# Kernel optimization log

Measured on AMD Instinct MI355X. Metric: run time of the kernel, lower is better.

The kernel has to match this reference:

```python
import jax, jax.numpy as jnp
import numpy as np

ATOM = 8          # atom_size
STRIDE = 4
NB_ATOMS = 256
LMBDA = 0.1       # l1 prox weight (prox_params)
NONDIFF = 20      # nondiff_steps (run under stop_gradient, mirroring torch.no_grad)
DIFF = 5          # diff_steps


def setup_inputs() -> dict:
    key = jax.random.key(0)
    k1, k2 = jax.random.split(key)
    y = jax.random.normal(k1, (8, 3, 256, 256), dtype=jnp.float32)
    # atoms ~ N(0,1)/sqrt(nb_channels*atom_size^2), as in __init__ with init='random'
    atoms = jax.random.normal(k2, (NB_ATOMS, 3, ATOM, ATOM), dtype=jnp.float32) / np.float32(np.sqrt(3 * ATOM * ATOM))
    return {"y": y, "atoms": atoms}


def _forward(y, atoms):
    B, C, H, W = y.shape
    a, s = ATOM, STRIDE
    Hp = (H - a) // s + 1
    Wp = (W - a) // s + 1
    D = C * a * a

    # patch row/col index grids: rows[ph, i] = ph*s + i
    rows = (jnp.arange(Hp) * s)[:, None] + jnp.arange(a)          # [Hp, a]
    cols = (jnp.arange(Wp) * s)[:, None] + jnp.arange(a)          # [Wp, a]
    R4 = rows[:, :, None, None]                                    # [Hp, a, 1, 1]
    C4 = cols[None, None, :, :]                                    # [1, 1, Wp, a]

    # unfold: extract overlapping patches -> [B, C, Hp, a, Wp, a] -> [N, D] (channel-major, matching torch)
    p6 = y[:, :, R4, C4]
    p = p6.transpose(0, 2, 4, 1, 3, 5).reshape(B * Hp * Wp, D)     # N = B*Hp*Wp

    mean = jnp.mean(p, axis=1, keepdims=True)                      # per-patch mean
    p = p - mean

    # l2-normalize atoms
    A = atoms.reshape(NB_ATOMS, D)
    A = A / jnp.linalg.norm(A, axis=1, keepdims=True)              # [nA, D]

    X = A @ A.T                                                    # [nA, nA] Gram matrix
    q = A @ p.T                                                    # [nA, N]
    L = jnp.linalg.norm(X, 2)                                      # spectral norm (Lipschitz const)
    thr = LMBDA / L

    def ista_step(c, _):
        c = c - (X @ c - q) / L
        c = jnp.sign(c) * jnp.maximum(jnp.abs(c) - thr, 0.0)       # soft-threshold prox
        return c, None

    c0 = jnp.zeros((NB_ATOMS, q.shape[1]), dtype=q.dtype)
    c, _ = jax.lax.scan(ista_step, c0, None, length=NONDIFF)
    c = jax.lax.stop_gradient(c)                                    # torch.no_grad() warmup
    c, _ = jax.lax.scan(ista_step, c, None, length=DIFF)

    # reconstruct patches: einsum('ij,il->jl') = c.T @ A, add mean back
    rec = c.T @ A + mean                                            # [N, D]
    p6r = rec.reshape(B, Hp, Wp, C, a, a).transpose(0, 3, 1, 4, 2, 5)  # [B, C, Hp, a, Wp, a]

    # fold: overlap-add patches back to image
    out = jnp.zeros((B, C, H, W), dtype=y.dtype).at[:, :, R4, C4].add(p6r)
    counts = jnp.zeros((H, W), dtype=y.dtype).at[R4, C4].add(
        jnp.ones((Hp, a, Wp, a), dtype=y.dtype))                    # overlap divisors
    return out / counts


def reference(y, atoms):
    return _forward(y, atoms)
```

## Files before the change

kernel.cpp:

```cpp
#include <hip/hip_runtime.h>
#include <math.h>

#define NPATCH 31752
#define TILE   64
#define PSTR   200
#define MSTR   200

typedef _Float16 f16;
typedef __attribute__((ext_vector_type(2))) _Float16 f16x2;
typedef __attribute__((ext_vector_type(4))) _Float16 f16x4;
typedef __attribute__((ext_vector_type(8))) _Float16 f16x8;
typedef __attribute__((ext_vector_type(2))) __fp16   hf16x2;
typedef __attribute__((ext_vector_type(4))) float    f32x4;
#define MFMA16 __builtin_amdgcn_mfma_f32_16x16x32_f16

union HU { f16x2 h; hf16x2 g; unsigned u; };

__device__ __forceinline__ f16x2 pk2(float a, float b)
{
    HU r; r.g = __builtin_amdgcn_cvt_pkrtz(a, b);
    return r.h;
}

__device__ __forceinline__ f16x2 shrink2(f16x2 v, f16x2 thr2)
{
    HU a; a.h = v;
    unsigned sgn = a.u & 0x80008000u;
    a.u &= 0x7FFF7FFFu;
    f16x2 t = a.h - thr2;
    t = __builtin_elementwise_max(t, (f16x2)(f16)0);
    HU r; r.h = t; r.u |= sgn;
    return r.h;
}

__global__ void fusedpack_kernel(const float* __restrict__ atoms,
                                 float* __restrict__ As,
                                 f16* __restrict__ Ap, f16* __restrict__ Ab,
                                 float* __restrict__ out, int out_n)
{
    __shared__ float part[6];
    const int b = blockIdx.x, t = threadIdx.x;
    {
        float4* o4 = (float4*)out;
        int tot4 = out_n >> 2;
        for (int u = b * 192 + t; u < tot4; u += 256 * 192)
            o4[u] = (float4){0.f, 0.f, 0.f, 0.f};
    }
    float v = atoms[b*192 + t];
    float s = v*v, r = v;
    #pragma unroll
    for (int m = 1; m < 64; m <<= 1) { s += __shfl_xor(s, m, 64); r += __shfl_xor(r, m, 64); }
    const int wv = t >> 6, lane = t & 63;
    if (lane == 0) { part[wv] = s; part[3 + wv] = r; }
    __syncthreads();
    s = part[0] + part[1] + part[2];
    r = part[3] + part[4] + part[5];
    float rn = 1.0f / sqrtf(s);
    float a  = v * rn;
    if (t == 0) As[b] = r * rn;
    f16 ah = (f16)a;
    {
        int I = b >> 4, l16 = b & 15;
        int ks = t >> 5, q = (t >> 3) & 3, j = t & 7;
        Ap[(((I*6 + ks)*64) + q*16 + l16)*8 + j] = ah;
    }
    {
        int dt = t >> 4, dl = t & 15;
        int ks = b >> 5, q = (b >> 3) & 3, j = b & 7;
        Ab[(((dt*8 + ks)*64) + q*16 + dl)*8 + j] = ah;
    }
    (void)lane;
}

__global__ __launch_bounds__(512, 1)
void lchain_kernel(const f16* __restrict__ Ab, const f16* __restrict__ Ap,
                   f16* __restrict__ Xp, float* __restrict__ scal)
{
    __shared__ __align__(16) f16 mls[2 * 192 * MSTR];
    __shared__ float red[8];
    __shared__ float trc[16];
    const int tid = threadIdx.x, bid = blockIdx.x;
    const int wv = tid >> 6, lane = tid & 63;
    const int quad = lane >> 4, l16 = lane & 15;

    if (bid > 0) {
        const int I = bid - 1;
        const f16x8* ApV = (const f16x8*)Ap;
        #pragma unroll
        for (int jj = 0; jj < 2; ++jj) {
            int J = wv*2 + jj;
            f32x4 acc = (f32x4){0,0,0,0};
            #pragma unroll
            for (int ks = 0; ks < 6; ++ks) {
                f16x8 af = ApV[(I*6 + ks)*64 + lane];
                f16x8 bf = ApV[(J*6 + ks)*64 + lane];
                acc = MFMA16(af, bf, acc, 0, 0, 0);
            }
            f16x2 lo = pk2(acc[0], acc[1]);
            f16x2 hi = pk2(acc[2], acc[3]);
            f16x4 cc; cc[0]=lo[0]; cc[1]=lo[1]; cc[2]=hi[0]; cc[3]=hi[1];
            int ks2 = I >> 1;
            int q2  = (2*I + (quad >> 1)) & 3;
            int j2  = (quad & 1) * 4;
            *(f16x4*)&Xp[(((J*8 + ks2)*64) + q2*16 + l16)*8 + j2] = cc;
        }
        return;
    }

    const int g3 = (wv >> 1) * 3;
    const int h6 = (wv & 1) * 6;
    const f16x8* AbV = (const f16x8*)Ab;

    f32x4 acc[3][6];
    #pragma unroll
    for (int it = 0; it < 3; ++it)
        #pragma unroll
        for (int jj = 0; jj < 6; ++jj) acc[it][jj] = (f32x4){0,0,0,0};
    for (int ks = 0; ks < 8; ++ks) {
        f16x8 bf[6];
        #pragma unroll
        for (int jj = 0; jj < 6; ++jj) bf[jj] = AbV[((h6 + jj)*8 + ks)*64 + lane];
        #pragma unroll
        for (int it = 0; it < 3; ++it) {
            f16x8 af = AbV[((g3 + it)*8 + ks)*64 + lane];
            #pragma unroll
            for (int jj = 0; jj < 6; ++jj)
                acc[it][jj] = MFMA16(af, bf[jj], acc[it][jj], 0, 0, 0);
        }
    }
    #pragma unroll
    for (int it = 0; it < 3; ++it) {
        int I = g3 + it;
        #pragma unroll
        for (int jj = 0; jj < 6; ++jj) {
            int J = h6 + jj;
            f16x2 lo = pk2(acc[it][jj][0], acc[it][jj][1]);
            f16x2 hi = pk2(acc[it][jj][2], acc[it][jj][3]);
            f16x4 cc; cc[0]=lo[0]; cc[1]=lo[1]; cc[2]=hi[0]; cc[3]=hi[1];
            *(f16x4*)&mls[(J*16 + l16)*MSTR + I*16 + quad*4] = cc;
        }
    }
    __syncthreads();

    float rprev = 1.0f;
    for (int t = 1; t <= 8; ++t) {
        const f16* src = mls + ((t & 1) ^ 1) * (192 * MSTR);
        f16*       dst = mls + (t & 1) * (192 * MSTR);
        const float inv = 1.0f / rprev;
        const float inv2 = inv * inv;

        f32x4 a2[3][6];
        #pragma unroll
        for (int it = 0; it < 3; ++it)
            #pragma unroll
            for (int jj = 0; jj < 6; ++jj) a2[it][jj] = (f32x4){0,0,0,0};
        for (int ksd = 0; ksd < 6; ++ksd) {
            f16x8 bf[6];
            #pragma unroll
            for (int jj = 0; jj < 6; ++jj)
                bf[jj] = *(const f16x8*)&src[((h6 + jj)*16 + l16)*MSTR + ksd*32 + quad*8];
            #pragma unroll
            for (int it = 0; it < 3; ++it) {
                f16x8 af = *(const f16x8*)&src[((g3 + it)*16 + l16)*MSTR + ksd*32 + quad*8];
                #pragma unroll
                for (int jj = 0; jj < 6; ++jj)
                    a2[it][jj] = MFMA16(af, bf[jj], a2[it][jj], 0, 0, 0);
            }
        }
        float dsum = 0.0f;
        #pragma unroll
        for (int it = 0; it < 3; ++it) {
            int I = g3 + it;
            #pragma unroll
            for (int jj = 0; jj < 6; ++jj) {
                int J = h6 + jj;
                float v0 = a2[it][jj][0] * inv2;
                float v1 = a2[it][jj][1] * inv2;
                float v2 = a2[it][jj][2] * inv2;
                float v3 = a2[it][jj][3] * inv2;
                f16x2 lo = pk2(v0, v1);
                f16x2 hi = pk2(v2, v3);
                f16x4 cc; cc[0]=lo[0]; cc[1]=lo[1]; cc[2]=hi[0]; cc[3]=hi[1];
                *(f16x4*)&dst[(J*16 + l16)*MSTR + I*16 + quad*4] = cc;
                if (J == I) {
                    int dg = l16 - quad*4;
                    if (dg >= 0 && dg < 4)
                        dsum += (dg == 0 ? v0 : dg == 1 ? v1 : dg == 2 ? v2 : v3);
                }
            }
        }
        #pragma unroll
        for (int m = 1; m < 64; m <<= 1) dsum += __shfl_xor(dsum, m, 64);
        if (lane == 0) red[wv] = dsum;
        __syncthreads();
        float r = red[0] + red[1] + red[2] + red[3]
                + red[4] + red[5] + red[6] + red[7];
        if (tid == 0) trc[t] = r;
        rprev = r;
        __syncthreads();
    }
    if (tid == 0) {
        float a = 0.0f;
        #pragma unroll
        for (int u = 1; u <= 8; ++u) a += exp2f(-(float)u) * log2f(trc[u]);
        float L = exp2f(a);
        scal[16] = 1.0f / L;
        scal[17] = 0.1f / L;
    }
}

__global__ __launch_bounds__(512, 4)
void mega_kernel(const float* __restrict__ y,
                 const f16* __restrict__ Xp, const f16* __restrict__ Ap,
                 const f16* __restrict__ Ab, const float* __restrict__ As,
                 const float* __restrict__ scal, float* __restrict__ out)
{
    __shared__ f16      p_lds[TILE * PSTR];
    __shared__ f16      c_lds[2 * 16 * 512];
    __shared__ float    mean_lds[TILE];
    __shared__ unsigned pco[TILE];

    const int tid  = threadIdx.x;
    const int base = blockIdx.x * TILE;
    const int wv = tid >> 6, lane = tid & 63, quad = lane >> 4, l16 = lane & 15;
    const float invL = scal[16];
    const float thr  = scal[17];
    const f16x2 thr2 = { (f16)thr, (f16)thr };

    #define CWADDR(st, rt, ct) \
        ((st)*8192 + ((ct)*8 + wv)*512 \
         + (((rt)*2 + (quad>>1))*16 + l16)*8 + (quad&1)*4)
    #define LDB0(st, ks) (*(const f16x8*)&c_lds[(st)*8192 + (ks)*512 + lane*8])
    #define LDB1(st, ks) (*(const f16x8*)&c_lds[(st)*8192 + (8 + (ks))*512 + lane*8])

    f16x8 greg[2][8];
    {
        const f16x8* XpV = (const f16x8*)Xp;
        #pragma unroll
        for (int rt = 0; rt < 2; ++rt) {
            int r = (wv*2 + rt)*16 + l16;
            #pragma unroll
            for (int ks = 0; ks < 8; ++ks) {
                f16x8 xv = XpV[((wv*2 + rt)*8 + ks)*64 + lane];
                float f[8];
                #pragma unroll
                for (int j = 0; j < 8; ++j) {
                    int c = ks*32 + quad*8 + j;
                    float d = (r == c) ? 1.0f : 0.0f;
                    f[j] = fmaf(-invL, (float)xv[j], d);
                }
                f16x2 p0 = pk2(f[0], f[1]), p1 = pk2(f[2], f[3]);
                f16x2 p2 = pk2(f[4], f[5]), p3 = pk2(f[6], f[7]);
                f16x8 gg;
                gg[0]=p0[0]; gg[1]=p0[1]; gg[2]=p1[0]; gg[3]=p1[1];
                gg[4]=p2[0]; gg[5]=p2[1]; gg[6]=p3[0]; gg[7]=p3[1];
                greg[rt][ks] = gg;
            }
        }
    }

    {
        int n_l = tid >> 3, qq = tid & 7;
        int n = base + n_l; if (n >= NPATCH) n = NPATCH - 1;
        int b = n / 3969, rem = n - b * 3969;
        int r = rem / 63, sc = rem - r * 63;
        float s = 0.0f;
        #pragma unroll
        for (int u = 0; u < 3; ++u) {
            int d  = qq * 24 + u * 8;
            int ch = d >> 6, id = (d & 63) >> 3;
            const float* src = &y[((b*3 + ch)*256 + (r*4 + id))*256 + sc*4];
            float4 a = *(const float4*)src;
            float4 bq = *(const float4*)(src + 4);
            s += a.x + a.y + a.z + a.w + bq.x + bq.y + bq.z + bq.w;
            f16x8 h = { (f16)a.x, (f16)a.y, (f16)a.z, (f16)a.w,
                        (f16)bq.x, (f16)bq.y, (f16)bq.z, (f16)bq.w };
            *(f16x8*)&p_lds[n_l * PSTR + d] = h;
        }
        s += __shfl_xor(s, 1, 64);
        s += __shfl_xor(s, 2, 64);
        s += __shfl_xor(s, 4, 64);
        if (qq == 0) {
            mean_lds[n_l] = s * (1.0f / 192.0f);
            pco[n_l] = ((unsigned)b << 16) | ((unsigned)r << 8) | (unsigned)sc;
        }
    }
    __syncthreads();

    f16x2 qslo[2][2][2], qshi[2][2][2];
    const f16x8* ApV = (const f16x8*)Ap;
    #pragma unroll
    for (int st = 0; st < 2; ++st) {
        f32x4 qf[2][2];
        #pragma unroll
        for (int rt = 0; rt < 2; ++rt)
            #pragma unroll
            for (int ct = 0; ct < 2; ++ct) qf[rt][ct] = (f32x4){0,0,0,0};
        #pragma unroll
        for (int ks = 0; ks < 6; ++ks) {
            f16x8 bf[2];
            #pragma unroll
            for (int ct = 0; ct < 2; ++ct)
                bf[ct] = *(const f16x8*)&p_lds[(st*32 + ct*16 + l16)*PSTR + ks*32 + quad*8];
            #pragma unroll
            for (int rt = 0; rt < 2; ++rt) {
                f16x8 af = ApV[((wv*2 + rt)*6 + ks)*64 + lane];
                #pragma unroll
                for (int ct = 0; ct < 2; ++ct)
                    qf[rt][ct] = MFMA16(af, bf[ct], qf[rt][ct], 0, 0, 0);
            }
        }
        #pragma unroll
        for (int rt = 0; rt < 2; ++rt) {
            float4 av = *(const float4*)&As[(wv*2 + rt)*16 + quad*4];
            #pragma unroll
            for (int ct = 0; ct < 2; ++ct) {
                float mn = mean_lds[st*32 + ct*16 + l16];
                float q0 = (qf[rt][ct][0] - mn*av.x) * invL;
                float q1 = (qf[rt][ct][1] - mn*av.y) * invL;
                float q2 = (qf[rt][ct][2] - mn*av.z) * invL;
                float q3 = (qf[rt][ct][3] - mn*av.w) * invL;
                f16x2 lo = pk2(q0, q1);
                f16x2 hi = pk2(q2, q3);
                qslo[st][rt][ct] = lo;  qshi[st][rt][ct] = hi;
                f16x2 clo = shrink2(lo, thr2);
                f16x2 chi = shrink2(hi, thr2);
                f16x4 cc; cc[0]=clo[0]; cc[1]=clo[1]; cc[2]=chi[0]; cc[3]=chi[1];
                *(f16x4*)&c_lds[CWADDR(st, rt, ct)] = cc;
            }
        }
    }
    __syncthreads();

    f16x8 pa0 = LDB0(0,0), pa1 = LDB1(0,0), pa2 = LDB0(0,1), pa3 = LDB1(0,1);
    for (int it = 0; it < 24; ++it) {
        f32x4 af[2][2];
        #pragma unroll
        for (int rt = 0; rt < 2; ++rt)
            #pragma unroll
            for (int ct = 0; ct < 2; ++ct) af[rt][ct] = (f32x4){0,0,0,0};
        __builtin_amdgcn_s_setprio(1);
        #pragma unroll
        for (int ks = 0; ks < 8; ++ks) {
            f16x8 b0 = (ks == 0) ? pa0 : (ks == 1) ? pa2 : LDB0(0, ks);
            f16x8 b1 = (ks == 0) ? pa1 : (ks == 1) ? pa3 : LDB1(0, ks);
            #pragma unroll
            for (int rt = 0; rt < 2; ++rt) {
                af[rt][0] = MFMA16(greg[rt][ks], b0, af[rt][0], 0, 0, 0);
                af[rt][1] = MFMA16(greg[rt][ks], b1, af[rt][1], 0, 0, 0);
            }
        }
        __builtin_amdgcn_s_setprio(0);
        __syncthreads();
        f16x8 pb0 = LDB0(1,0), pb1 = LDB1(1,0), pb2 = LDB0(1,1), pb3 = LDB1(1,1);
        #pragma unroll
        for (int rt = 0; rt < 2; ++rt)
            #pragma unroll
            for (int ct = 0; ct < 2; ++ct) {
                f16x2 vlo = pk2(af[rt][ct][0], af[rt][ct][1]) + qslo[0][rt][ct];
                f16x2 vhi = pk2(af[rt][ct][2], af[rt][ct][3]) + qshi[0][rt][ct];
                vlo = shrink2(vlo, thr2);
                vhi = shrink2(vhi, thr2);
                f16x4 cc; cc[0]=vlo[0]; cc[1]=vlo[1]; cc[2]=vhi[0]; cc[3]=vhi[1];
                *(f16x4*)&c_lds[CWADDR(0, rt, ct)] = cc;
            }
        #pragma unroll
        for (int rt = 0; rt < 2; ++rt)
            #pragma unroll
            for (int ct = 0; ct < 2; ++ct) af[rt][ct] = (f32x4){0,0,0,0};
        __builtin_amdgcn_s_setprio(1);
        #pragma unroll
        for (int ks = 0; ks < 8; ++ks) {
            f16x8 b0 = (ks == 0) ? pb0 : (ks == 1) ? pb2 : LDB0(1, ks);
            f16x8 b1 = (ks == 0) ? pb1 : (ks == 1) ? pb3 : LDB1(1, ks);
            #pragma unroll
            for (int rt = 0; rt < 2; ++rt) {
                af[rt][0] = MFMA16(greg[rt][ks], b0, af[rt][0], 0, 0, 0);
                af[rt][1] = MFMA16(greg[rt][ks], b1, af[rt][1], 0, 0, 0);
            }
        }
        __builtin_amdgcn_s_setprio(0);
        __syncthreads();
        pa0 = LDB0(0,0); pa1 = LDB1(0,0); pa2 = LDB0(0,1); pa3 = LDB1(0,1);
        #pragma unroll
        for (int rt = 0; rt < 2; ++rt)
            #pragma unroll
            for (int ct = 0; ct < 2; ++ct) {
                f16x2 vlo = pk2(af[rt][ct][0], af[rt][ct][1]) + qslo[1][rt][ct];
                f16x2 vhi = pk2(af[rt][ct][2], af[rt][ct][3]) + qshi[1][rt][ct];
                vlo = shrink2(vlo, thr2);
                vhi = shrink2(vhi, thr2);
                f16x4 cc; cc[0]=vlo[0]; cc[1]=vlo[1]; cc[2]=vhi[0]; cc[3]=vhi[1];
                *(f16x4*)&c_lds[CWADDR(1, rt, ct)] = cc;
            }
    }
    __syncthreads();

    const int nt = wv >> 2, dtb = 3 * (wv & 3);
    const f16x8* AbV = (const f16x8*)Ab;
    #pragma unroll
    for (int st = 0; st < 2; ++st) {
        f32x4 rf[3];
        #pragma unroll
        for (int u = 0; u < 3; ++u) rf[u] = (f32x4){0,0,0,0};
        #pragma unroll
        for (int ks = 0; ks < 8; ++ks) {
            f16x8 afr = *(const f16x8*)&c_lds[st*8192 + (nt*8 + ks)*512 + lane*8];
            #pragma unroll
            for (int u = 0; u < 3; ++u) {
                f16x8 bb = AbV[((dtb + u)*8 + ks)*64 + lane];
                rf[u] = MFMA16(afr, bb, rf[u], 0, 0, 0);
            }
        }
        #pragma unroll
        for (int g = 0; g < 4; ++g) {
            int nl = nt*16 + quad*4 + g;
            int n  = base + st*32 + nl;
            if (n < NPATCH) {
                unsigned pc = pco[st*32 + nl];
                int b = pc >> 16, r = (pc >> 8) & 255, sc = pc & 255;
                float mn = mean_lds[st*32 + nl];
                #pragma unroll
                for (int u = 0; u < 3; ++u) {
                    int d  = (dtb + u)*16 + l16;
                    int ch = d >> 6, dh = (d & 63) >> 3, dw = d & 7;
                    int h  = r*4 + dh, w2 = sc*4 + dw;
                    int cnth = min(62, h >> 2)  - (max(h - 4, 0) >> 2) + 1;
                    int cntw = min(62, w2 >> 2) - (max(w2 - 4, 0) >> 2) + 1;
                    float rcp = 1.0f / (float)(cnth * cntw);
                    atomicAdd(&out[((b*3 + ch)*256 + (r*4 + dh))*256 + sc*4 + dw],
                              (rf[u][g] + mn) * rcp);
                }
            }
        }
    }
    #undef CWADDR
    #undef LDB0
    #undef LDB1
}

extern "C" void kernel_launch(void* const* d_in, const int* in_sizes, int n_in,
                              void* d_out, int out_size, void* d_ws, size_t ws_size,
                              hipStream_t stream)
{
    const float* y     = (const float*)d_in[0];
    const float* atoms = (const float*)d_in[1];
    float* out = (float*)d_out;
    float* ws  = (float*)d_ws;

    float* As   = ws + 49152;
    float* scal = ws + 49408;
    f16*   Ap   = (f16*)(ws + 49440);
    f16*   Ab   = (f16*)(ws + 74016);
    f16*   Xp   = (f16*)(ws + 98592);
    int    outn = out_size;

    fusedpack_kernel<<<256, 192, 0, stream>>>(atoms, As, Ap, Ab, out, outn);
    lchain_kernel   <<<17, 512,  0, stream>>>(Ab, Ap, Xp, scal);
    mega_kernel     <<<(NPATCH + TILE - 1) / TILE, 512, 0, stream>>>
        (y, Xp, Ap, Ab, As, scal, out);
}
```

Before: 195.1 us.

## Fuse spectral-norm chain and Gram kernel into mega kernel via device flags

Removes the separate lchain kernel launch. Its work now runs in an extra block of the main kernel: block 497 runs the power/trace chain and publishes 1/L through a release-stored flag, and blocks 0-15 compute the Gram tiles and bump an atomic counter. Other blocks load patches first, then spin-wait on the flag and counter before building the ISTA iteration matrix. This overlaps the serial L computation with patch loading and removes a launch boundary. It risks a deadlock if the chain block is not scheduled while other blocks spin, and the chain block now reuses one LDS buffer with an extra barrier instead of double buffering.

```diff
diff --git a/kernel.cpp b/kernel.cpp
--- a/kernel.cpp
+++ b/kernel.cpp
@@ -5,6 +5,8 @@
 #define TILE   64
 #define PSTR   200
 #define MSTR   200
+#define CHAIN_BID 497
+#define FLAG_MAGIC 0xC0FFEE01ull
 
 typedef _Float16 f16;
 typedef __attribute__((ext_vector_type(2))) _Float16 f16x2;
@@ -15,6 +17,7 @@
 #define MFMA16 __builtin_amdgcn_mfma_f32_16x16x32_f16
 
 union HU { f16x2 h; hf16x2 g; unsigned u; };
+union FU { float f; unsigned u; };
 
 __device__ __forceinline__ f16x2 pk2(float a, float b)
 {
@@ -36,10 +39,15 @@
 __global__ void fusedpack_kernel(const float* __restrict__ atoms,
                                  float* __restrict__ As,
                                  f16* __restrict__ Ap, f16* __restrict__ Ab,
+                                 float* __restrict__ scal,
                                  float* __restrict__ out, int out_n)
 {
     __shared__ float part[6];
     const int b = blockIdx.x, t = threadIdx.x;
+    if (b == 0 && t == 0) {
+        *(unsigned long long*)&scal[20] = 0ull;
+        *(unsigned*)&scal[22] = 0u;
+    }
     {
         float4* o4 = (float4*)out;
         int tot4 = out_n >> 2;
@@ -69,22 +77,135 @@
         int ks = b >> 5, q = (b >> 3) & 3, j = b & 7;
         Ab[(((dt*8 + ks)*64) + q*16 + dl)*8 + j] = ah;
     }
-    (void)lane;
 }
 
-__global__ __launch_bounds__(512, 1)
-void lchain_kernel(const f16* __restrict__ Ab, const f16* __restrict__ Ap,
-                   f16* __restrict__ Xp, float* __restrict__ scal)
+__global__ __launch_bounds__(512, 4)
+void mega_kernel(const float* __restrict__ y, f16* __restrict__ Xp,
+                 const f16* __restrict__ Ap, const f16* __restrict__ Ab,
+                 const float* __restrict__ As, float* __restrict__ scal,
+                 float* __restrict__ out)
 {
-    __shared__ __align__(16) f16 mls[2 * 192 * MSTR];
+    __shared__ __align__(16) unsigned char smem[76800];
     __shared__ float red[8];
     __shared__ float trc[16];
+    __shared__ float bc_invL;
+
+    f16*      p_lds    = (f16*)smem;
+    f16*      c_lds    = (f16*)(smem + 25600);
+    float*    mean_lds = (float*)(smem + 58368);
+    unsigned* pco      = (unsigned*)(smem + 58624);
+
     const int tid = threadIdx.x, bid = blockIdx.x;
-    const int wv = tid >> 6, lane = tid & 63;
-    const int quad = lane >> 4, l16 = lane & 15;
-
-    if (bid > 0) {
-        const int I = bid - 1;
+    const int wv = tid >> 6, lane = tid & 63, quad = lane >> 4, l16 = lane & 15;
+
+    if (bid == CHAIN_BID) {
+        f16* mM = (f16*)smem;
+        const int g3 = (wv >> 1) * 3;
+        const int h6 = (wv & 1) * 6;
+        const f16x8* AbV = (const f16x8*)Ab;
+        f32x4 acc[3][6];
+        #pragma unroll
+        for (int it = 0; it < 3; ++it)
+            #pragma unroll
+            for (int jj = 0; jj < 6; ++jj) acc[it][jj] = (f32x4){0,0,0,0};
+        for (int ks = 0; ks < 8; ++ks) {
+            f16x8 bf[6];
+            #pragma unroll
+            for (int jj = 0; jj < 6; ++jj) bf[jj] = AbV[((h6 + jj)*8 + ks)*64 + lane];
+            #pragma unroll
+            for (int it = 0; it < 3; ++it) {
+                f16x8 af = AbV[((g3 + it)*8 + ks)*64 + lane];
+                #pragma unroll
+                for (int jj = 0; jj < 6; ++jj)
+                    acc[it][jj] = MFMA16(af, bf[jj], acc[it][jj], 0, 0, 0);
+            }
+        }
+        #pragma unroll
+        for (int it = 0; it < 3; ++it) {
+            int I = g3 + it;
+            #pragma unroll
+            for (int jj = 0; jj < 6; ++jj) {
+                int J = h6 + jj;
+                f16x2 lo = pk2(acc[it][jj][0], acc[it][jj][1]);
+                f16x2 hi = pk2(acc[it][jj][2], acc[it][jj][3]);
+                f16x4 cc; cc[0]=lo[0]; cc[1]=lo[1]; cc[2]=hi[0]; cc[3]=hi[1];
+                *(f16x4*)&mM[(J*16 + l16)*MSTR + I*16 + quad*4] = cc;
+            }
+        }
+        __syncthreads();
+
+        float rprev = 1.0f;
+        for (int t = 1; t <= 8; ++t) {
+            const float inv = 1.0f / rprev;
+            const float inv2 = inv * inv;
+            f32x4 a2[3][6];
+            #pragma unroll
+            for (int it = 0; it < 3; ++it)
+                #pragma unroll
+                for (int jj = 0; jj < 6; ++jj) a2[it][jj] = (f32x4){0,0,0,0};
+            for (int ksd = 0; ksd < 6; ++ksd) {
+                f16x8 bf[6];
+                #pragma unroll
+                for (int jj = 0; jj < 6; ++jj)
+                    bf[jj] = *(const f16x8*)&mM[((h6 + jj)*16 + l16)*MSTR + ksd*32 + quad*8];
+                #pragma unroll
+                for (int it = 0; it < 3; ++it) {
+                    f16x8 af = *(const f16x8*)&mM[((g3 + it)*16 + l16)*MSTR + ksd*32 + quad*8];
+                    #pragma unroll
+                    for (int jj = 0; jj < 6; ++jj)
+                        a2[it][jj] = MFMA16(af, bf[jj], a2[it][jj], 0, 0, 0);
+                }
+            }
+            __syncthreads();
+            float dsum = 0.0f;
+            #pragma unroll
+            for (int it = 0; it < 3; ++it) {
+                int I = g3 + it;
+                #pragma unroll
+                for (int jj = 0; jj < 6; ++jj) {
+                    int J = h6 + jj;
+                    float v0 = a2[it][jj][0] * inv2;
+                    float v1 = a2[it][jj][1] * inv2;
+                    float v2 = a2[it][jj][2] * inv2;
+                    float v3 = a2[it][jj][3] * inv2;
+                    f16x2 lo = pk2(v0, v1);
+                    f16x2 hi = pk2(v2, v3);
+                    f16x4 cc; cc[0]=lo[0]; cc[1]=lo[1]; cc[2]=hi[0]; cc[3]=hi[1];
+                    *(f16x4*)&mM[(J*16 + l16)*MSTR + I*16 + quad*4] = cc;
+                    if (J == I) {
+                        int dg = l16 - quad*4;
+                        if (dg >= 0 && dg < 4)
+                            dsum += (dg == 0 ? v0 : dg == 1 ? v1 : dg == 2 ? v2 : v3);
+                    }
+                }
+            }
+            #pragma unroll
+            for (int m = 1; m < 64; m <<= 1) dsum += __shfl_xor(dsum, m, 64);
+            if (lane == 0) red[wv] = dsum;
+            __syncthreads();
+            float r = red[0] + red[1] + red[2] + red[3]
+                    + red[4] + red[5] + red[6] + red[7];
+            if (tid == 0) trc[t] = r;
+            rprev = r;
+            __syncthreads();
+        }
+        if (tid == 0) {
+            float a = 0.0f;
+            #pragma unroll
+            for (int u = 1; u <= 8; ++u) a += exp2f(-(float)u) * log2f(trc[u]);
+            float L = exp2f(a);
+            FU cv; cv.f = 1.0f / L;
+            unsigned long long pk = (FLAG_MAGIC << 32) | (unsigned long long)cv.u;
+            __hip_atomic_store((unsigned long long*)&scal[20], pk,
+                               __ATOMIC_RELEASE, __HIP_MEMORY_SCOPE_AGENT);
+        }
+        return;
+    }
+
+    const int base = bid * TILE;
+
+    if (bid < 16) {
+        const int I = bid;
         const f16x8* ApV = (const f16x8*)Ap;
         #pragma unroll
         for (int jj = 0; jj < 2; ++jj) {
@@ -104,158 +225,11 @@
             int j2  = (quad & 1) * 4;
             *(f16x4*)&Xp[(((J*8 + ks2)*64) + q2*16 + l16)*8 + j2] = cc;
         }
-        return;
-    }
-
-    const int g3 = (wv >> 1) * 3;
-    const int h6 = (wv & 1) * 6;
-    const f16x8* AbV = (const f16x8*)Ab;
-
-    f32x4 acc[3][6];
-    #pragma unroll
-    for (int it = 0; it < 3; ++it)
-        #pragma unroll
-        for (int jj = 0; jj < 6; ++jj) acc[it][jj] = (f32x4){0,0,0,0};
-    for (int ks = 0; ks < 8; ++ks) {
-        f16x8 bf[6];
-        #pragma unroll
-        for (int jj = 0; jj < 6; ++jj) bf[jj] = AbV[((h6 + jj)*8 + ks)*64 + lane];
-        #pragma unroll
-        for (int it = 0; it < 3; ++it) {
-            f16x8 af = AbV[((g3 + it)*8 + ks)*64 + lane];
-            #pragma unroll
-            for (int jj = 0; jj < 6; ++jj)
-                acc[it][jj] = MFMA16(af, bf[jj], acc[it][jj], 0, 0, 0);
-        }
-    }
-    #pragma unroll
-    for (int it = 0; it < 3; ++it) {
-        int I = g3 + it;
-        #pragma unroll
-        for (int jj = 0; jj < 6; ++jj) {
-            int J = h6 + jj;
-            f16x2 lo = pk2(acc[it][jj][0], acc[it][jj][1]);
-            f16x2 hi = pk2(acc[it][jj][2], acc[it][jj][3]);
-            f16x4 cc; cc[0]=lo[0]; cc[1]=lo[1]; cc[2]=hi[0]; cc[3]=hi[1];
-            *(f16x4*)&mls[(J*16 + l16)*MSTR + I*16 + quad*4] = cc;
-        }
-    }
-    __syncthreads();
-
-    float rprev = 1.0f;
-    for (int t = 1; t <= 8; ++t) {
-        const f16* src = mls + ((t & 1) ^ 1) * (192 * MSTR);
-        f16*       dst = mls + (t & 1) * (192 * MSTR);
-        const float inv = 1.0f / rprev;
-        const float inv2 = inv * inv;
-
-        f32x4 a2[3][6];
-        #pragma unroll
-        for (int it = 0; it < 3; ++it)
-            #pragma unroll
-            for (int jj = 0; jj < 6; ++jj) a2[it][jj] = (f32x4){0,0,0,0};
-        for (int ksd = 0; ksd < 6; ++ksd) {
-            f16x8 bf[6];
-            #pragma unroll
-            for (int jj = 0; jj < 6; ++jj)
-                bf[jj] = *(const f16x8*)&src[((h6 + jj)*16 + l16)*MSTR + ksd*32 + quad*8];
-            #pragma unroll
-            for (int it = 0; it < 3; ++it) {
-                f16x8 af = *(const f16x8*)&src[((g3 + it)*16 + l16)*MSTR + ksd*32 + quad*8];
-                #pragma unroll
-                for (int jj = 0; jj < 6; ++jj)
-                    a2[it][jj] = MFMA16(af, bf[jj], a2[it][jj], 0, 0, 0);
-            }
-        }
-        float dsum = 0.0f;
-        #pragma unroll
-        for (int it = 0; it < 3; ++it) {
-            int I = g3 + it;
-            #pragma unroll
-            for (int jj = 0; jj < 6; ++jj) {
-                int J = h6 + jj;
-                float v0 = a2[it][jj][0] * inv2;
-                float v1 = a2[it][jj][1] * inv2;
-                float v2 = a2[it][jj][2] * inv2;
-                float v3 = a2[it][jj][3] * inv2;
-                f16x2 lo = pk2(v0, v1);
-                f16x2 hi = pk2(v2, v3);
-                f16x4 cc; cc[0]=lo[0]; cc[1]=lo[1]; cc[2]=hi[0]; cc[3]=hi[1];
-                *(f16x4*)&dst[(J*16 + l16)*MSTR + I*16 + quad*4] = cc;
-                if (J == I) {
-                    int dg = l16 - quad*4;
-                    if (dg >= 0 && dg < 4)
-                        dsum += (dg == 0 ? v0 : dg == 1 ? v1 : dg == 2 ? v2 : v3);
-                }
-            }
-        }
-        #pragma unroll
-        for (int m = 1; m < 64; m <<= 1) dsum += __shfl_xor(dsum, m, 64);
-        if (lane == 0) red[wv] = dsum;
         __syncthreads();
-        float r = red[0] + red[1] + red[2] + red[3]
-                + red[4] + red[5] + red[6] + red[7];
-        if (tid == 0) trc[t] = r;
-        rprev = r;
-        __syncthreads();
-    }
-    if (tid == 0) {
-        float a = 0.0f;
-        #pragma unroll
-        for (int u = 1; u <= 8; ++u) a += exp2f(-(float)u) * log2f(trc[u]);
-        float L = exp2f(a);
-        scal[16] = 1.0f / L;
-        scal[17] = 0.1f / L;
-    }
-}
-
-__global__ __launch_bounds__(512, 4)
-void mega_kernel(const float* __restrict__ y,
-                 const f16* __restrict__ Xp, const f16* __restrict__ Ap,
-                 const f16* __restrict__ Ab, const float* __restrict__ As,
-                 const float* __restrict__ scal, float* __restrict__ out)
-{
-    __shared__ f16      p_lds[TILE * PSTR];
-    __shared__ f16      c_lds[2 * 16 * 512];
-    __shared__ float    mean_lds[TILE];
-    __shared__ unsigned pco[TILE];
-
-    const int tid  = threadIdx.x;
-    const int base = blockIdx.x * TILE;
-    const int wv = tid >> 6, lane = tid & 63, quad = lane >> 4, l16 = lane & 15;
-    const float invL = scal[16];
-    const float thr  = scal[17];
-    const f16x2 thr2 = { (f16)thr, (f16)thr };
-
-    #define CWADDR(st, rt, ct) \
-        ((st)*8192 + ((ct)*8 + wv)*512 \
-         + (((rt)*2 + (quad>>1))*16 + l16)*8 + (quad&1)*4)
-    #define LDB0(st, ks) (*(const f16x8*)&c_lds[(st)*8192 + (ks)*512 + lane*8])
-    #define LDB1(st, ks) (*(const f16x8*)&c_lds[(st)*8192 + (8 + (ks))*512 + lane*8])
-
-    f16x8 greg[2][8];
-    {
-        const f16x8* XpV = (const f16x8*)Xp;
-        #pragma unroll
-        for (int rt = 0; rt < 2; ++rt) {
-            int r = (wv*2 + rt)*16 + l16;
-            #pragma unroll
-            for (int ks = 0; ks < 8; ++ks) {
-                f16x8 xv = XpV[((wv*2 + rt)*8 + ks)*64 + lane];
-                float f[8];
-                #pragma unroll
-                for (int j = 0; j < 8; ++j) {
-                    int c = ks*32 + quad*8 + j;
-                    float d = (r == c) ? 1.0f : 0.0f;
-                    f[j] = fmaf(-invL, (float)xv[j], d);
-                }
-                f16x2 p0 = pk2(f[0], f[1]), p1 = pk2(f[2], f[3]);
-                f16x2 p2 = pk2(f[4], f[5]), p3 = pk2(f[6], f[7]);
-                f16x8 gg;
-                gg[0]=p0[0]; gg[1]=p0[1]; gg[2]=p1[0]; gg[3]=p1[1];
-                gg[4]=p2[0]; gg[5]=p2[1]; gg[6]=p3[0]; gg[7]=p3[1];
-                greg[rt][ks] = gg;
-            }
+        if (tid == 0) {
+            __threadfence();
+            __hip_atomic_fetch_add((unsigned*)&scal[22], 1u,
+                                   __ATOMIC_RELEASE, __HIP_MEMORY_SCOPE_AGENT);
         }
     }
 
@@ -286,6 +260,26 @@
         }
     }
     __syncthreads();
+
+    if (tid == 0) {
+        unsigned long long v;
+        while (((v = __hip_atomic_load((unsigned long long*)&scal[20],
+                                       __ATOMIC_ACQUIRE, __HIP_MEMORY_SCOPE_AGENT))
+                >> 32) != FLAG_MAGIC)
+            __builtin_amdgcn_s_sleep(8);
+        FU cv; cv.u = (unsigned)(v & 0xFFFFFFFFull);
+        bc_invL = cv.f;
+    }
+    __syncthreads();
+    const float invL = bc_invL;
+    const float thr  = 0.1f * invL;
+    const f16x2 thr2 = { (f16)thr, (f16)thr };
+
+    #define CWADDR(st, rt, ct) \
+        ((st)*8192 + ((ct)*8 + wv)*512 \
+         + (((rt)*2 + (quad>>1))*16 + l16)*8 + (quad&1)*4)
+    #define LDB0(st, ks) (*(const f16x8*)&c_lds[(st)*8192 + (ks)*512 + lane*8])
+    #define LDB1(st, ks) (*(const f16x8*)&c_lds[(st)*8192 + (8 + (ks))*512 + lane*8])
 
     f16x2 qslo[2][2][2], qshi[2][2][2];
     const f16x8* ApV = (const f16x8*)Ap;
@@ -332,6 +326,39 @@
     }
     __syncthreads();
 
+    if (tid == 0) {
+        while (__hip_atomic_load((unsigned*)&scal[22],
+                                 __ATOMIC_ACQUIRE, __HIP_MEMORY_SCOPE_AGENT) < 16u)
+            __builtin_amdgcn_s_sleep(8);
+    }
+    __syncthreads();
+
+    f16x8 greg[2][8];
+    {
+        const f16x8* XpV = (const f16x8*)Xp;
+        #pragma unroll
+        for (int rt = 0; rt < 2; ++rt) {
+            int r = (wv*2 + rt)*16 + l16;
+            #pragma unroll
+            for (int ks = 0; ks < 8; ++ks) {
+                f16x8 xv = XpV[((wv*2 + rt)*8 + ks)*64 + lane];
+                float f[8];
+                #pragma unroll
+                for (int j = 0; j < 8; ++j) {
+                    int c = ks*32 + quad*8 + j;
+                    float d = (r == c) ? 1.0f : 0.0f;
+                    f[j] = fmaf(-invL, (float)xv[j], d);
+                }
+                f16x2 p0 = pk2(f[0], f[1]), p1 = pk2(f[2], f[3]);
+                f16x2 p2 = pk2(f[4], f[5]), p3 = pk2(f[6], f[7]);
+                f16x8 gg;
+                gg[0]=p0[0]; gg[1]=p0[1]; gg[2]=p1[0]; gg[3]=p1[1];
+                gg[4]=p2[0]; gg[5]=p2[1]; gg[6]=p3[0]; gg[7]=p3[1];
+                greg[rt][ks] = gg;
+            }
+        }
+    }
+
     f16x8 pa0 = LDB0(0,0), pa1 = LDB1(0,0), pa2 = LDB0(0,1), pa3 = LDB1(0,1);
     for (int it = 0; it < 24; ++it) {
         f32x4 af[2][2];
@@ -455,8 +482,7 @@
     f16*   Xp   = (f16*)(ws + 98592);
     int    outn = out_size;
 
-    fusedpack_kernel<<<256, 192, 0, stream>>>(atoms, As, Ap, Ab, out, outn);
-    lchain_kernel   <<<17, 512,  0, stream>>>(Ab, Ap, Xp, scal);
-    mega_kernel     <<<(NPATCH + TILE - 1) / TILE, 512, 0, stream>>>
+    fusedpack_kernel<<<256, 192, 0, stream>>>(atoms, As, Ap, Ab, scal, out, outn);
+    mega_kernel     <<<CHAIN_BID + 1, 512, 0, stream>>>
         (y, Xp, Ap, Ab, As, scal, out);
 }
```

Measured after the change: 445.6 us. +128.4%, slower.

## Fuse atom normalization/packing into spectral-norm chain kernel, dropping a launch

Applied to the files above, without the earlier changes.

Merges the atom normalize/pack kernel and the Gram/power-chain kernel into one prep kernel. Gram blocks and the trace-chain block each renormalize the atoms themselves into LDS instead of reading packed copies from global memory, so there is no dependency between the two former launches. The other blocks still emit As/Ap/Ab for the main kernel. This removes one kernel launch and its global round trip, at the cost of redundant normalization work and a larger LDS footprint (147 KB) in the chain block, which now squares the Gram matrix in place.

```diff
diff --git a/kernel.cpp b/kernel.cpp
--- a/kernel.cpp
+++ b/kernel.cpp
@@ -33,59 +33,95 @@
     return r.h;
 }
 
-__global__ void fusedpack_kernel(const float* __restrict__ atoms,
-                                 float* __restrict__ As,
-                                 f16* __restrict__ Ap, f16* __restrict__ Ab,
-                                 float* __restrict__ out, int out_n)
+__global__ __launch_bounds__(512, 1)
+void prep_kernel(const float* __restrict__ atoms,
+                 float* __restrict__ As, f16* __restrict__ Ap,
+                 f16* __restrict__ Ab, f16* __restrict__ Xp,
+                 float* __restrict__ scal,
+                 float* __restrict__ out, int out_n)
 {
+    __shared__ __align__(16) unsigned char smem[147456];
+    __shared__ float red[8];
+    __shared__ float trc[16];
     __shared__ float part[6];
-    const int b = blockIdx.x, t = threadIdx.x;
+
+    const int tid = threadIdx.x, bid = blockIdx.x;
+    const int wv = tid >> 6, lane = tid & 63;
+    const int quad = lane >> 4, l16 = lane & 15;
+
     {
         float4* o4 = (float4*)out;
         int tot4 = out_n >> 2;
-        for (int u = b * 192 + t; u < tot4; u += 256 * 192)
+        for (int u = bid * 512 + tid; u < tot4; u += 273 * 512)
             o4[u] = (float4){0.f, 0.f, 0.f, 0.f};
     }
-    float v = atoms[b*192 + t];
-    float s = v*v, r = v;
-    #pragma unroll
-    for (int m = 1; m < 64; m <<= 1) { s += __shfl_xor(s, m, 64); r += __shfl_xor(r, m, 64); }
-    const int wv = t >> 6, lane = t & 63;
-    if (lane == 0) { part[wv] = s; part[3 + wv] = r; }
-    __syncthreads();
-    s = part[0] + part[1] + part[2];
-    r = part[3] + part[4] + part[5];
-    float rn = 1.0f / sqrtf(s);
-    float a  = v * rn;
-    if (t == 0) As[b] = r * rn;
-    f16 ah = (f16)a;
-    {
-        int I = b >> 4, l16 = b & 15;
-        int ks = t >> 5, q = (t >> 3) & 3, j = t & 7;
-        Ap[(((I*6 + ks)*64) + q*16 + l16)*8 + j] = ah;
-    }
-    {
-        int dt = t >> 4, dl = t & 15;
-        int ks = b >> 5, q = (b >> 3) & 3, j = b & 7;
-        Ab[(((dt*8 + ks)*64) + q*16 + dl)*8 + j] = ah;
-    }
-    (void)lane;
-}
-
-__global__ __launch_bounds__(512, 1)
-void lchain_kernel(const f16* __restrict__ Ab, const f16* __restrict__ Ap,
-                   f16* __restrict__ Xp, float* __restrict__ scal)
-{
-    __shared__ __align__(16) f16 mls[2 * 192 * MSTR];
-    __shared__ float red[8];
-    __shared__ float trc[16];
-    const int tid = threadIdx.x, bid = blockIdx.x;
-    const int wv = tid >> 6, lane = tid & 63;
-    const int quad = lane >> 4, l16 = lane & 15;
-
-    if (bid > 0) {
+
+    if (bid >= 17) {
+        const int b = bid - 17;
+        float v = 0.0f;
+        if (tid < 192) v = atoms[b*192 + tid];
+        float s = v*v, r = v;
+        #pragma unroll
+        for (int m = 1; m < 64; m <<= 1) { s += __shfl_xor(s, m, 64); r += __shfl_xor(r, m, 64); }
+        if (lane == 0 && wv < 3) { part[wv] = s; part[3 + wv] = r; }
+        __syncthreads();
+        if (tid < 192) {
+            float ss = part[0] + part[1] + part[2];
+            float rr = part[3] + part[4] + part[5];
+            float rn = 1.0f / sqrtf(ss);
+            float a  = v * rn;
+            if (tid == 0) As[b] = rr * rn;
+            f16 ah = (f16)a;
+            {
+                int I = b >> 4, l16b = b & 15;
+                int ks = tid >> 5, q = (tid >> 3) & 3, j = tid & 7;
+                Ap[(((I*6 + ks)*64) + q*16 + l16b)*8 + j] = ah;
+            }
+            {
+                int dt = tid >> 4, dl = tid & 15;
+                int ks = b >> 5, q = (b >> 3) & 3, j = b & 7;
+                Ab[(((dt*8 + ks)*64) + q*16 + dl)*8 + j] = ah;
+            }
+        }
+        return;
+    }
+
+    float* stg  = (float*)smem;
+    float4* stg4 = (float4*)smem;
+
+    if (bid >= 1) {
         const int I = bid - 1;
-        const f16x8* ApV = (const f16x8*)Ap;
+        f16* Apf = (f16*)(smem + 49152);
+        for (int c = 0; c < 4; ++c) {
+            __syncthreads();
+            const float4* src4 = (const float4*)(atoms + c * 64 * 192);
+            #pragma unroll
+            for (int k = 0; k < 6; ++k) stg4[tid + k*512] = src4[tid + k*512];
+            __syncthreads();
+            #pragma unroll
+            for (int rr = 0; rr < 8; ++rr) {
+                int lr = wv*8 + rr;
+                int b  = c*64 + lr;
+                float v0 = stg[lr*192 + lane];
+                float v1 = stg[lr*192 +  64 + lane];
+                float v2 = stg[lr*192 + 128 + lane];
+                float s = v0*v0 + v1*v1 + v2*v2;
+                #pragma unroll
+                for (int m = 1; m < 64; m <<= 1) s += __shfl_xor(s, m, 64);
+                float rn = 1.0f / sqrtf(s);
+                const int Ib = b >> 4, l16b = b & 15;
+                float vv[3] = { v0, v1, v2 };
+                #pragma unroll
+                for (int u = 0; u < 3; ++u) {
+                    int t = u*64 + lane;
+                    f16 ah = (f16)(vv[u] * rn);
+                    int ks = t >> 5, q = (t >> 3) & 3, j = t & 7;
+                    Apf[(((Ib*6 + ks)*64) + q*16 + l16b)*8 + j] = ah;
+                }
+            }
+        }
+        __syncthreads();
+        const f16x8* ApV = (const f16x8*)Apf;
         #pragma unroll
         for (int jj = 0; jj < 2; ++jj) {
             int J = wv*2 + jj;
@@ -107,105 +143,142 @@
         return;
     }
 
-    const int g3 = (wv >> 1) * 3;
-    const int h6 = (wv & 1) * 6;
-    const f16x8* AbV = (const f16x8*)Ab;
-
-    f32x4 acc[3][6];
-    #pragma unroll
-    for (int it = 0; it < 3; ++it)
-        #pragma unroll
-        for (int jj = 0; jj < 6; ++jj) acc[it][jj] = (f32x4){0,0,0,0};
-    for (int ks = 0; ks < 8; ++ks) {
-        f16x8 bf[6];
-        #pragma unroll
-        for (int jj = 0; jj < 6; ++jj) bf[jj] = AbV[((h6 + jj)*8 + ks)*64 + lane];
-        #pragma unroll
-        for (int it = 0; it < 3; ++it) {
-            f16x8 af = AbV[((g3 + it)*8 + ks)*64 + lane];
-            #pragma unroll
-            for (int jj = 0; jj < 6; ++jj)
-                acc[it][jj] = MFMA16(af, bf[jj], acc[it][jj], 0, 0, 0);
-        }
-    }
-    #pragma unroll
-    for (int it = 0; it < 3; ++it) {
-        int I = g3 + it;
-        #pragma unroll
-        for (int jj = 0; jj < 6; ++jj) {
-            int J = h6 + jj;
-            f16x2 lo = pk2(acc[it][jj][0], acc[it][jj][1]);
-            f16x2 hi = pk2(acc[it][jj][2], acc[it][jj][3]);
-            f16x4 cc; cc[0]=lo[0]; cc[1]=lo[1]; cc[2]=hi[0]; cc[3]=hi[1];
-            *(f16x4*)&mls[(J*16 + l16)*MSTR + I*16 + quad*4] = cc;
-        }
-    }
-    __syncthreads();
-
-    float rprev = 1.0f;
-    for (int t = 1; t <= 8; ++t) {
-        const f16* src = mls + ((t & 1) ^ 1) * (192 * MSTR);
-        f16*       dst = mls + (t & 1) * (192 * MSTR);
-        const float inv = 1.0f / rprev;
-        const float inv2 = inv * inv;
-
-        f32x4 a2[3][6];
+    {
+        f16* Abf = (f16*)(smem + 49152);
+        const int g3 = (wv >> 1) * 3;
+        const int h6 = (wv & 1) * 6;
+
+        f32x4 acc[3][6];
         #pragma unroll
         for (int it = 0; it < 3; ++it)
             #pragma unroll
-            for (int jj = 0; jj < 6; ++jj) a2[it][jj] = (f32x4){0,0,0,0};
-        for (int ksd = 0; ksd < 6; ++ksd) {
-            f16x8 bf[6];
-            #pragma unroll
-            for (int jj = 0; jj < 6; ++jj)
-                bf[jj] = *(const f16x8*)&src[((h6 + jj)*16 + l16)*MSTR + ksd*32 + quad*8];
-            #pragma unroll
-            for (int it = 0; it < 3; ++it) {
-                f16x8 af = *(const f16x8*)&src[((g3 + it)*16 + l16)*MSTR + ksd*32 + quad*8];
+            for (int jj = 0; jj < 6; ++jj) acc[it][jj] = (f32x4){0,0,0,0};
+
+        for (int h = 0; h < 2; ++h) {
+            for (int c = 0; c < 2; ++c) {
+                __syncthreads();
+                const float4* src4 = (const float4*)(atoms + (h*128 + c*64) * 192);
+                #pragma unroll
+                for (int k = 0; k < 6; ++k) stg4[tid + k*512] = src4[tid + k*512];
+                __syncthreads();
+                #pragma unroll
+                for (int rr = 0; rr < 8; ++rr) {
+                    int lr  = wv*8 + rr;
+                    int lbh = c*64 + lr;
+                    float v0 = stg[lr*192 + lane];
+                    float v1 = stg[lr*192 +  64 + lane];
+                    float v2 = stg[lr*192 + 128 + lane];
+                    float s = v0*v0 + v1*v1 + v2*v2;
+                    #pragma unroll
+                    for (int m = 1; m < 64; m <<= 1) s += __shfl_xor(s, m, 64);
+                    float rn = 1.0f / sqrtf(s);
+                    const int ksb = lbh >> 5, qb = (lbh >> 3) & 3, jb = lbh & 7;
+                    float vv[3] = { v0, v1, v2 };
+                    #pragma unroll
+                    for (int u = 0; u < 3; ++u) {
+                        int t = u*64 + lane;
+                        f16 ah = (f16)(vv[u] * rn);
+                        int dt = t >> 4, dl = t & 15;
+                        Abf[(((dt*4 + ksb)*64) + qb*16 + dl)*8 + jb] = ah;
+                    }
+                }
+            }
+            __syncthreads();
+            const f16x8* AbV = (const f16x8*)Abf;
+            for (int ksl = 0; ksl < 4; ++ksl) {
+                f16x8 bf[6];
                 #pragma unroll
                 for (int jj = 0; jj < 6; ++jj)
-                    a2[it][jj] = MFMA16(af, bf[jj], a2[it][jj], 0, 0, 0);
-            }
-        }
-        float dsum = 0.0f;
+                    bf[jj] = AbV[((h6 + jj)*4 + ksl)*64 + lane];
+                #pragma unroll
+                for (int it = 0; it < 3; ++it) {
+                    f16x8 af = AbV[((g3 + it)*4 + ksl)*64 + lane];
+                    #pragma unroll
+                    for (int jj = 0; jj < 6; ++jj)
+                        acc[it][jj] = MFMA16(af, bf[jj], acc[it][jj], 0, 0, 0);
+                }
+            }
+        }
+        __syncthreads();
+
+        f16* mM = (f16*)smem;
         #pragma unroll
         for (int it = 0; it < 3; ++it) {
             int I = g3 + it;
             #pragma unroll
             for (int jj = 0; jj < 6; ++jj) {
                 int J = h6 + jj;
-                float v0 = a2[it][jj][0] * inv2;
-                float v1 = a2[it][jj][1] * inv2;
-                float v2 = a2[it][jj][2] * inv2;
-                float v3 = a2[it][jj][3] * inv2;
-                f16x2 lo = pk2(v0, v1);
-                f16x2 hi = pk2(v2, v3);
+                f16x2 lo = pk2(acc[it][jj][0], acc[it][jj][1]);
+                f16x2 hi = pk2(acc[it][jj][2], acc[it][jj][3]);
                 f16x4 cc; cc[0]=lo[0]; cc[1]=lo[1]; cc[2]=hi[0]; cc[3]=hi[1];
-                *(f16x4*)&dst[(J*16 + l16)*MSTR + I*16 + quad*4] = cc;
-                if (J == I) {
-                    int dg = l16 - quad*4;
-                    if (dg >= 0 && dg < 4)
-                        dsum += (dg == 0 ? v0 : dg == 1 ? v1 : dg == 2 ? v2 : v3);
-                }
-            }
-        }
-        #pragma unroll
-        for (int m = 1; m < 64; m <<= 1) dsum += __shfl_xor(dsum, m, 64);
-        if (lane == 0) red[wv] = dsum;
+                *(f16x4*)&mM[(J*16 + l16)*MSTR + I*16 + quad*4] = cc;
+            }
+        }
         __syncthreads();
-        float r = red[0] + red[1] + red[2] + red[3]
-                + red[4] + red[5] + red[6] + red[7];
-        if (tid == 0) trc[t] = r;
-        rprev = r;
-        __syncthreads();
-    }
-    if (tid == 0) {
-        float a = 0.0f;
-        #pragma unroll
-        for (int u = 1; u <= 8; ++u) a += exp2f(-(float)u) * log2f(trc[u]);
-        float L = exp2f(a);
-        scal[16] = 1.0f / L;
-        scal[17] = 0.1f / L;
+
+        float rprev = 1.0f;
+        for (int t = 1; t <= 8; ++t) {
+            const float inv = 1.0f / rprev;
+            const float inv2 = inv * inv;
+            f32x4 a2[3][6];
+            #pragma unroll
+            for (int it = 0; it < 3; ++it)
+                #pragma unroll
+                for (int jj = 0; jj < 6; ++jj) a2[it][jj] = (f32x4){0,0,0,0};
+            for (int ksd = 0; ksd < 6; ++ksd) {
+                f16x8 bf[6];
+                #pragma unroll
+                for (int jj = 0; jj < 6; ++jj)
+                    bf[jj] = *(const f16x8*)&mM[((h6 + jj)*16 + l16)*MSTR + ksd*32 + quad*8];
+                #pragma unroll
+                for (int it = 0; it < 3; ++it) {
+                    f16x8 af = *(const f16x8*)&mM[((g3 + it)*16 + l16)*MSTR + ksd*32 + quad*8];
+                    #pragma unroll
+                    for (int jj = 0; jj < 6; ++jj)
+                        a2[it][jj] = MFMA16(af, bf[jj], a2[it][jj], 0, 0, 0);
+                }
+            }
+            __syncthreads();
+            float dsum = 0.0f;
+            #pragma unroll
+            for (int it = 0; it < 3; ++it) {
+                int I = g3 + it;
+                #pragma unroll
+                for (int jj = 0; jj < 6; ++jj) {
+                    int J = h6 + jj;
+                    float v0 = a2[it][jj][0] * inv2;
+                    float v1 = a2[it][jj][1] * inv2;
+                    float v2 = a2[it][jj][2] * inv2;
+                    float v3 = a2[it][jj][3] * inv2;
+                    f16x2 lo = pk2(v0, v1);
+                    f16x2 hi = pk2(v2, v3);
+                    f16x4 cc; cc[0]=lo[0]; cc[1]=lo[1]; cc[2]=hi[0]; cc[3]=hi[1];
+                    *(f16x4*)&mM[(J*16 + l16)*MSTR + I*16 + quad*4] = cc;
+                    if (J == I) {
+                        int dg = l16 - quad*4;
+                        if (dg >= 0 && dg < 4)
+                            dsum += (dg == 0 ? v0 : dg == 1 ? v1 : dg == 2 ? v2 : v3);
+                    }
+                }
+            }
+            #pragma unroll
+            for (int m = 1; m < 64; m <<= 1) dsum += __shfl_xor(dsum, m, 64);
+            if (lane == 0) red[wv] = dsum;
+            __syncthreads();
+            float r = red[0] + red[1] + red[2] + red[3]
+                    + red[4] + red[5] + red[6] + red[7];
+            if (tid == 0) trc[t] = r;
+            rprev = r;
+            __syncthreads();
+        }
+        if (tid == 0) {
+            float a = 0.0f;
+            #pragma unroll
+            for (int u = 1; u <= 8; ++u) a += exp2f(-(float)u) * log2f(trc[u]);
+            float L = exp2f(a);
+            scal[16] = 1.0f / L;
+            scal[17] = 0.1f / L;
+        }
     }
 }
 
@@ -455,8 +528,7 @@
     f16*   Xp   = (f16*)(ws + 98592);
     int    outn = out_size;
 
-    fusedpack_kernel<<<256, 192, 0, stream>>>(atoms, As, Ap, Ab, out, outn);
-    lchain_kernel   <<<17, 512,  0, stream>>>(Ab, Ap, Xp, scal);
-    mega_kernel     <<<(NPATCH + TILE - 1) / TILE, 512, 0, stream>>>
+    prep_kernel<<<273, 512, 0, stream>>>(atoms, As, Ap, Ab, Xp, scal, out, outn);
+    mega_kernel<<<(NPATCH + TILE - 1) / TILE, 512, 0, stream>>>
         (y, Xp, Ap, Ab, As, scal, out);
 }
```

After: 206.6 us. 1.06x slower.
